# Optimization experiments

Measured on AMD Instinct MI355X. Metric: run time of the kernel, lower is better.

The kernel has to match this reference:

```python
import jax, jax.numpy as jnp
import numpy as np

C = 64          # out_C
IN_C = 2 * C    # in_C
B, H, W = 4, 64, 64


def conv_bn_relu(x, w, s, b):
    # 3x3 conv (stride 1, pad 1, no bias) + folded BatchNorm affine + ReLU
    y = jax.lax.conv_general_dilated(
        x, w, window_strides=(1, 1), padding=((1, 1), (1, 1)),
        dimension_numbers=("NCHW", "OIHW", "NCHW"))
    return jax.nn.relu(y * s[None, :, None, None] + b[None, :, None, None])


def attend(K, V, Q):
    # K, V, Q: [B, C, H, W]; mask = softmax(K^T Q) over last dim; out = V @ mask^T
    b, c, h, w = V.shape
    n = h * w
    Kf = K.reshape(b, c, n)
    Vf = V.reshape(b, c, n)
    Qf = Q.reshape(b, c, n)
    mask = jax.nn.softmax(jnp.einsum("bcn,bcm->bnm", Kf, Qf), axis=-1)  # [B,N,N]
    ref = jnp.einsum("bcn,bmn->bcm", Vf, mask)                          # V @ mask^T
    return ref.reshape(b, c, h, w)


def _conv_params(key, cin, cout):
    k1, k2, k3 = jax.random.split(key, 3)
    w = jax.random.normal(k1, (cout, cin, 3, 3), jnp.float32) * (1.0 / np.sqrt(cin * 9))
    s = jax.random.uniform(k2, (cout,), jnp.float32, 0.5, 1.5)   # folded BN scale
    bb = jax.random.normal(k3, (cout,), jnp.float32) * 0.1       # folded BN shift
    return w, s, bb


def setup_inputs() -> dict:
    key = jax.random.key(0)
    ks = jax.random.split(key, 9)
    x = jax.random.normal(ks[0], (B, C, H, W), jnp.float32)
    y = jax.random.normal(ks[1], (B, C, H, W), jnp.float32)
    q_w, q_s, q_b = _conv_params(ks[2], IN_C, C)
    rk_w, rk_s, rk_b = _conv_params(ks[3], C, C)
    rv_w, rv_s, rv_b = _conv_params(ks[4], C, C)
    ik_w, ik_s, ik_b = _conv_params(ks[5], C, C)
    iv_w, iv_s, iv_b = _conv_params(ks[6], C, C)
    sr_w, sr_s, sr_b = _conv_params(ks[7], IN_C, C)
    g1 = jax.random.normal(jax.random.fold_in(ks[8], 1), (1,), jnp.float32) * 0.1
    g2 = jax.random.normal(jax.random.fold_in(ks[8], 2), (1,), jnp.float32) * 0.1
    return dict(x=x, y=y,
                q_w=q_w, q_s=q_s, q_b=q_b,
                rk_w=rk_w, rk_s=rk_s, rk_b=rk_b,
                rv_w=rv_w, rv_s=rv_s, rv_b=rv_b,
                ik_w=ik_w, ik_s=ik_s, ik_b=ik_b,
                iv_w=iv_w, iv_s=iv_s, iv_b=iv_b,
                sr_w=sr_w, sr_s=sr_s, sr_b=sr_b,
                gamma1=g1, gamma2=g2)


def reference(x, y, q_w, q_s, q_b, rk_w, rk_s, rk_b, rv_w, rv_s, rv_b,
              ik_w, ik_s, ik_b, iv_w, iv_s, iv_b, sr_w, sr_s, sr_b,
              gamma1, gamma2):
    Q = conv_bn_relu(jnp.concatenate([x, y], axis=1), q_w, q_s, q_b)
    rgb_k = conv_bn_relu(x, rk_w, rk_s, rk_b)
    rgb_v = conv_bn_relu(x, rv_w, rv_s, rv_b)
    rgb_refine = gamma1[0] * attend(rgb_k, rgb_v, Q) + y
    inf_k = conv_bn_relu(y, ik_w, ik_s, ik_b)
    inf_v = conv_bn_relu(y, iv_w, iv_s, iv_b)
    inf_refine = gamma2[0] * attend(inf_k, inf_v, Q) + x
    out = conv_bn_relu(jnp.concatenate([rgb_refine, inf_refine], axis=1), sr_w, sr_s, sr_b)
    return out
```

## Files before the change

kernel.cpp:

```cpp
#include <hip/hip_runtime.h>
#include <hip/hip_bf16.h>

#define NPOS 4096
#define CD   64
#define NB   4
#define PADW 66
#define PADN (66*66)
#define NSEG 4
#define NT   (NPOS / NSEG / 64)
#define LOG2E 1.4426950408889634f

extern "C" __device__ float __ocml_exp2_f32(float);

typedef __bf16 bf16x8_t __attribute__((ext_vector_type(8)));
typedef float  f32x4_t  __attribute__((ext_vector_type(4)));

static __device__ __forceinline__ unsigned short f2bf(float f) {
    return __builtin_bit_cast(unsigned short, __float2bfloat16(f));
}

static __device__ __forceinline__ void gload_lds16(const void* g, void* l) {
    __builtin_amdgcn_global_load_lds(
        (const __attribute__((address_space(1))) void*)g,
        (__attribute__((address_space(3))) void*)l, 16, 0, 0);
}

static __device__ __forceinline__ unsigned cvtpk_bf16(float lo, float hi) {
    unsigned r;
    asm("v_cvt_pk_bf16_f32 %0, %1, %2" : "=v"(r) : "v"(lo), "v"(hi));
    return r;
}

__global__ __launch_bounds__(256) void prep_kernel(
    const float* __restrict__ x, const float* __restrict__ y,
    const float* __restrict__ qw, const float* __restrict__ rkw,
    const float* __restrict__ rvw, const float* __restrict__ ikw,
    const float* __restrict__ ivw, const float* __restrict__ srw,
    const float* __restrict__ qs, const float* __restrict__ rks,
    const float* __restrict__ rvs, const float* __restrict__ iks,
    const float* __restrict__ ivs, const float* __restrict__ srs,
    unsigned short* __restrict__ pads, unsigned short* __restrict__ Wf)
{
    const int bx = blockIdx.x;
    if (bx < 16) {
        unsigned short* p = pads + (size_t)bx * PADN * CD;
        const uint4 z = make_uint4(0, 0, 0, 0);
        for (int idx = threadIdx.x; idx < 260 * 8; idx += 256) {
            const int pi = idx >> 3, chn = idx & 7;
            int pos;
            if (pi < 66)       pos = pi;
            else if (pi < 132) pos = 65 * PADW + (pi - 66);
            else { const int rem = pi - 132;
                   pos = (1 + (rem >> 1)) * PADW + ((rem & 1) ? 65 : 0); }
            *(uint4*)(p + (size_t)pos * CD + chn * 8) = z;
        }
        return;
    }
    if (bx < 160) {
        const int f = bx - 16;
        const float* w; const float* s; int cin, local;
        if (f < 36)       { w = qw;  s = qs;  cin = 128; local = f; }
        else if (f < 54)  { w = rkw; s = rks; cin = 64;  local = f - 36; }
        else if (f < 72)  { w = rvw; s = rvs; cin = 64;  local = f - 54; }
        else if (f < 90)  { w = ikw; s = iks; cin = 64;  local = f - 72; }
        else if (f < 108) { w = ivw; s = ivs; cin = 64;  local = f - 90; }
        else              { w = srw; s = srs; cin = 128; local = f - 108; }
        const int src = (cin == 128) ? local / 18 : 0;
        const int rem = (cin == 128) ? local % 18 : local;
        const int tap = rem >> 1, kt = rem & 1;
        const int t = threadIdx.x, cot = t >> 6, l = t & 63;
        const int co = cot * 16 + (l & 15);
        const float kmul = ((f >= 36 && f < 54) || (f >= 72 && f < 90)) ? LOG2E : 1.0f;
        const float sc = s[co] * kmul;
        unsigned short us[8];
#pragma unroll
        for (int e = 0; e < 8; ++e) {
            const int ci = src * 64 + kt * 32 + ((l >> 4) * 8) + e;
            us[e] = f2bf(w[((size_t)co * cin + ci) * 9 + tap] * sc);
        }
        *(uint4*)(Wf + ((size_t)(f * 4 + cot) * 64 + l) * 8) = *(uint4*)us;
        return;
    }
    {
        const int idx = bx - 160;
        const int h = idx & 63, b = (idx >> 6) & 3, src = idx >> 8;
        const float* in = src ? y : x;
        unsigned short* out = pads + (size_t)src * NB * PADN * CD;
        __shared__ float t[64][65];
        const int tt = threadIdx.x;
        {
            const int ci = tt >> 2, w0 = (tt & 3) * 16;
            const float* p = in + ((size_t)b * 64 + ci) * NPOS + h * 64 + w0;
#pragma unroll
            for (int j = 0; j < 16; j += 4) {
                float4 v = *(const float4*)(p + j);
                t[ci][w0 + j] = v.x; t[ci][w0 + j + 1] = v.y;
                t[ci][w0 + j + 2] = v.z; t[ci][w0 + j + 3] = v.w;
            }
        }
        __syncthreads();
        const int w = tt >> 2, c0 = (tt & 3) * 16;
        unsigned short us[16];
#pragma unroll
        for (int j = 0; j < 16; ++j) us[j] = f2bf(t[c0 + j][w]);
        unsigned short* q = out + ((size_t)b * PADN + (h + 1) * PADW + (w + 1)) * CD + c0;
        *(uint4*)q = *(uint4*)us;
        *(uint4*)(q + 8) = *(uint4*)(us + 8);
    }
}

__global__ __launch_bounds__(256) void conv_mfma_kernel(
    const unsigned short* __restrict__ xpad, const unsigned short* __restrict__ ypad,
    const unsigned short* __restrict__ rpadR, const unsigned short* __restrict__ rpadI,
    const unsigned short* __restrict__ Wf,
    const float* __restrict__ qb, const float* __restrict__ rkb,
    const float* __restrict__ rvb, const float* __restrict__ ikb,
    const float* __restrict__ ivb, const float* __restrict__ srb,
    unsigned short* __restrict__ Qt, unsigned short* __restrict__ KtR,
    unsigned short* __restrict__ VR, unsigned short* __restrict__ KtI,
    unsigned short* __restrict__ VI, float* __restrict__ outf,
    int convid_base)
{
    const int conv = convid_base + (blockIdx.z >> 1);
    const int ch   = blockIdx.z & 1;
    const int hg = blockIdx.x, b = blockIdx.y;
    const unsigned short *in0, *in1; const float* bias;
    int nsrc, wfbase, layout; void* outp;
    switch (conv) {
        case 0:  in0 = xpad;  in1 = ypad;  nsrc = 2; wfbase = 0;   bias = qb;  outp = Qt;  layout = 0; break;
        case 1:  in0 = xpad;  in1 = 0;     nsrc = 1; wfbase = 36;  bias = rkb; outp = KtR; layout = 0; break;
        case 2:  in0 = xpad;  in1 = 0;     nsrc = 1; wfbase = 54;  bias = rvb; outp = VR;  layout = 1; break;
        case 3:  in0 = ypad;  in1 = 0;     nsrc = 1; wfbase = 72;  bias = ikb; outp = KtI; layout = 0; break;
        case 4:  in0 = ypad;  in1 = 0;     nsrc = 1; wfbase = 90;  bias = ivb; outp = VI;  layout = 1; break;
        default: in0 = rpadR; in1 = rpadI; nsrc = 2; wfbase = 108; bias = srb; outp = outf; layout = 2; break;
    }
    const float bmul = (conv == 1 || conv == 3) ? LOG2E : 1.0f;
    const int tid = threadIdx.x;
    const int lane = tid & 63, wv = tid >> 6;
    const int l15 = lane & 15, g = lane >> 4;
    const int rr = wv >> 1;
    const int wseg = (wv & 1) * 32;

    __shared__ unsigned short As[264 * 64];
    __shared__ unsigned short Wl[36 * 512];

    f32x4_t acc[2][2];
#pragma unroll
    for (int i = 0; i < 2; ++i)
#pragma unroll
        for (int j = 0; j < 2; ++j) acc[i][j] = (f32x4_t){0.f, 0.f, 0.f, 0.f};

    for (int src = 0; src < nsrc; ++src) {
        if (src) __syncthreads();
        const unsigned short* tsrc =
            (src ? in1 : in0) + ((size_t)b * PADN + (size_t)hg * 2 * PADW) * CD;
        for (int k = 0; k < 2112; k += 256) {
            const int idx = k + tid;
            if (idx < 2112) {
                const int s = (idx & ~7) | ((idx ^ (idx >> 3)) & 7);
                gload_lds16(tsrc + (size_t)s * 8, As + (size_t)(idx & ~63) * 8);
            }
        }
#pragma unroll
        for (int j = 0; j < 9; ++j) {
            const int slot = wv * 9 + j;
            const int fg = wfbase + src * 18 + (slot >> 1);
            gload_lds16(Wf + ((size_t)(fg * 4 + ch * 2 + (slot & 1)) * 64 + lane) * 8,
                        Wl + slot * 512);
        }
        __syncthreads();
#pragma unroll
        for (int ky = 0; ky < 3; ++ky) {
#pragma unroll
            for (int kx = 0; kx < 3; ++kx) {
#pragma unroll
                for (int kt = 0; kt < 2; ++kt) {
                    const int fj = (ky * 3 + kx) * 2 + kt;
                    bf16x8_t a[2];
#pragma unroll
                    for (int pf = 0; pf < 2; ++pf) {
                        const int P = (rr + ky) * 66 + wseg + pf * 16 + kx + l15;
                        const int q = (kt * 4 + g) ^ (P & 7);
                        a[pf] = *(const bf16x8_t*)(As + P * 64 + q * 8);
                    }
#pragma unroll
                    for (int cc = 0; cc < 2; ++cc) {
                        bf16x8_t wfr = *(const bf16x8_t*)(Wl + (size_t)(fj * 2 + cc) * 512 + lane * 8);
                        acc[0][cc] = __builtin_amdgcn_mfma_f32_16x16x32_bf16(a[0], wfr, acc[0][cc], 0, 0, 0);
                        acc[1][cc] = __builtin_amdgcn_mfma_f32_16x16x32_bf16(a[1], wfr, acc[1][cc], 0, 0, 0);
                    }
                }
            }
        }
    }

    const int hrow = hg * 2 + rr;
#pragma unroll
    for (int pf = 0; pf < 2; ++pf) {
        const int nb4 = hrow * 64 + wseg + pf * 16 + g * 4;
        if (layout == 0) {
            unsigned short* o = (unsigned short*)outp + (size_t)b * NPOS * CD;
#pragma unroll
            for (int cc = 0; cc < 2; ++cc) {
                const int co = (ch * 2 + cc) * 16 + l15;
                const float bv = bias[co] * bmul;
#pragma unroll
                for (int r = 0; r < 4; ++r)
                    o[(size_t)(nb4 + r) * CD + co] = f2bf(fmaxf(acc[pf][cc][r] + bv, 0.f));
            }
        } else if (layout == 1) {
            unsigned short* o = (unsigned short*)outp + (size_t)b * CD * NPOS;
#pragma unroll
            for (int cc = 0; cc < 2; ++cc) {
                const int cch = (ch * 2 + cc) * 16 + l15;
                const float bv = bias[cch];
                unsigned short us[4];
#pragma unroll
                for (int r = 0; r < 4; ++r) us[r] = f2bf(fmaxf(acc[pf][cc][r] + bv, 0.f));
                *(uint2*)(o + (size_t)cch * NPOS + nb4) = *(uint2*)us;
            }
        } else {
            float* o = (float*)outp + (size_t)b * CD * NPOS;
#pragma unroll
            for (int cc = 0; cc < 2; ++cc) {
                const int cch = (ch * 2 + cc) * 16 + l15;
                const float bv = bias[cch];
                f32x4_t v;
#pragma unroll
                for (int r = 0; r < 4; ++r) v[r] = fmaxf(acc[pf][cc][r] + bv, 0.f);
                *(f32x4_t*)(o + (size_t)cch * NPOS + nb4) = v;
            }
        }
    }
}

__global__ __launch_bounds__(256) void attn_kernel(
    const unsigned short* __restrict__ Qt,
    const unsigned short* __restrict__ KtR, const unsigned short* __restrict__ KtI,
    const unsigned short* __restrict__ VR,  const unsigned short* __restrict__ VI,
    float* __restrict__ Opart, float* __restrict__ ml)
{
    const int fid = blockIdx.x;
    const int att = fid & 1;
    const int b   = (fid >> 1) & 3;
    const int seg = (fid >> 3) & 3;
    const int mblk = fid >> 5;
    const int lane = threadIdx.x & 63, wv = threadIdx.x >> 6;
    const int l15 = lane & 15, g = lane >> 4;
    const int m0 = mblk * 64 + wv * 16;

    const unsigned short* Qb = Qt + (size_t)b * NPOS * CD;
    const unsigned short* Kb = (att ? KtI : KtR) + (size_t)b * NPOS * CD;
    const unsigned short* Vb = (att ? VI : VR) + (size_t)b * CD * NPOS;

    __shared__ unsigned short Qs[2][64 * 64];
    __shared__ unsigned short Vs[2][64 * 64];
    __shared__ unsigned short plds[4][16 * 68];
    unsigned short* pl = plds[wv];

    const bf16x8_t bK0 = *(const bf16x8_t*)&Kb[(size_t)(m0 + l15) * CD + g * 8];
    const bf16x8_t bK1 = *(const bf16x8_t*)&Kb[(size_t)(m0 + l15) * CD + 32 + g * 8];

    f32x4_t O[4];
#pragma unroll
    for (int i = 0; i < 4; ++i) O[i] = (f32x4_t){0.f, 0.f, 0.f, 0.f};
    float mrun = -3.0e38f, lsum = 0.f;

    const int csw = (lane & 7) ^ ((lane >> 3) & 7);
    const int sx = l15 & 7;
    const int nbase = seg * (NPOS / NSEG);

    const int rq = wv * 16 + (lane >> 3);
    const unsigned short* qsrc0 = Qb + (size_t)(nbase + rq) * CD + csw * 8;
    const unsigned short* qsrc1 = qsrc0 + (size_t)8 * CD;
    const unsigned short* vsrc0 = Vb + (size_t)rq * NPOS + nbase + csw * 8;
    const unsigned short* vsrc1 = vsrc0 + (size_t)8 * NPOS;
    unsigned short* qdst = &Qs[0][(wv * 16) * 64];
    unsigned short* vdst = &Vs[0][(wv * 16) * 64];

#define STAGE(buf, itv) do {                                                  \
        const size_t qo = (size_t)(itv) * (64 * CD);                          \
        const size_t vo = (size_t)(itv) * 64;                                 \
        gload_lds16(qsrc0 + qo, qdst + (buf) * 4096);                         \
        gload_lds16(qsrc1 + qo, qdst + (buf) * 4096 + 512);                   \
        gload_lds16(vsrc0 + vo, vdst + (buf) * 4096);                         \
        gload_lds16(vsrc1 + vo, vdst + (buf) * 4096 + 512);                   \
    } while (0)

    STAGE(0, 0);

    for (int it = 0; it < NT; ++it) {
        const int cur = it & 1;
        __syncthreads();
        if (it + 1 < NT) STAGE(cur ^ 1, it + 1);

        f32x4_t St[4];
        __builtin_amdgcn_s_setprio(1);
#pragma unroll
        for (int nt = 0; nt < 4; ++nt) {
            const unsigned short* qr = &Qs[cur][(nt * 16 + l15) * 64];
            bf16x8_t a0 = *(const bf16x8_t*)(qr + (g ^ sx) * 8);
            bf16x8_t a1 = *(const bf16x8_t*)(qr + ((4 + g) ^ sx) * 8);
            f32x4_t c = (f32x4_t){0.f, 0.f, 0.f, 0.f};
            c = __builtin_amdgcn_mfma_f32_16x16x32_bf16(a0, bK0, c, 0, 0, 0);
            c = __builtin_amdgcn_mfma_f32_16x16x32_bf16(a1, bK1, c, 0, 0, 0);
            St[nt] = c;
        }
        __builtin_amdgcn_s_setprio(0);

        float tmax = St[0][0];
#pragma unroll
        for (int nt = 0; nt < 4; ++nt) {
            tmax = fmaxf(fmaxf(tmax, St[nt][0]), St[nt][1]);
            tmax = fmaxf(fmaxf(tmax, St[nt][2]), St[nt][3]);
        }
        if (!__all(tmax <= mrun + 12.0f)) {
            float tr = fmaxf(tmax, __shfl_xor(tmax, 16));
            tr = fmaxf(tr, __shfl_xor(tr, 32));
            const float mnew = fmaxf(mrun, tr);
            const float corr = __builtin_amdgcn_exp2f(mrun - mnew);
            lsum *= corr;
#pragma unroll
            for (int i = 0; i < 4; ++i) {
                O[i][0] *= corr; O[i][1] *= corr; O[i][2] *= corr; O[i][3] *= corr;
            }
            mrun = mnew;
        }
        unsigned int pw[8];
#pragma unroll
        for (int nt = 0; nt < 4; ++nt) {
            float p0 = __builtin_amdgcn_exp2f(St[nt][0] - mrun);
            float p1 = __builtin_amdgcn_exp2f(St[nt][1] - mrun);
            float p2 = __builtin_amdgcn_exp2f(St[nt][2] - mrun);
            float p3 = __builtin_amdgcn_exp2f(St[nt][3] - mrun);
            lsum += (p0 + p1) + (p2 + p3);
            pw[nt * 2 + 0] = cvtpk_bf16(p0, p1);
            pw[nt * 2 + 1] = cvtpk_bf16(p2, p3);
        }
#pragma unroll
        for (int nt = 0; nt < 4; ++nt)
            *(uint2*)&pl[l15 * 68 + nt * 16 + g * 4] =
                make_uint2(pw[nt * 2], pw[nt * 2 + 1]);

        __builtin_amdgcn_s_setprio(1);
#pragma unroll
        for (int nc = 0; nc < 2; ++nc) {
            union { bf16x8_t v; uint2 d2[2]; } bp;
            bp.d2[0] = *(uint2*)&pl[l15 * 68 + nc * 32 + g * 8];
            bp.d2[1] = *(uint2*)&pl[l15 * 68 + nc * 32 + g * 8 + 4];
#pragma unroll
            for (int ct = 0; ct < 4; ++ct) {
                bf16x8_t av = *(const bf16x8_t*)
                    (&Vs[cur][(ct * 16 + l15) * 64 + (((nc * 4 + g) ^ sx) * 8)]);
                O[ct] = __builtin_amdgcn_mfma_f32_16x16x32_bf16(av, bp.v, O[ct], 0, 0, 0);
            }
        }
        __builtin_amdgcn_s_setprio(0);
    }

    float lred = lsum + __shfl_xor(lsum, 16);
    lred += __shfl_xor(lred, 32);
    float* Ob = Opart + ((((size_t)att * NB + b) * NSEG + seg) * NPOS) * CD;
    const int m = m0 + l15;
#pragma unroll
    for (int ct = 0; ct < 4; ++ct)
        *(f32x4_t*)(Ob + (size_t)m * CD + ct * 16 + g * 4) = O[ct];
    if (g == 0) {
        float* mlb = ml + ((((size_t)att * NB + b) * NSEG + seg) * NPOS + m) * 2;
        mlb[0] = mrun; mlb[1] = lred;
    }
#undef STAGE
}

__global__ __launch_bounds__(256) void combine_kernel(
    const float* __restrict__ Opart, const float* __restrict__ ml,
    const float* __restrict__ x, const float* __restrict__ y,
    const float* __restrict__ g1, const float* __restrict__ g2,
    unsigned short* __restrict__ rpadR, unsigned short* __restrict__ rpadI)
{
    const int mt = blockIdx.x, b = blockIdx.y, att = blockIdx.z;
    const float* resid = att ? x : y;
    const float gamma = att ? g2[0] : g1[0];
    unsigned short* rp = (att ? rpadI : rpadR) + (size_t)b * PADN * CD;
    __shared__ float t[64][17];
    const int tt = threadIdx.x;
    {
        const int c = tt >> 2, m4 = (tt & 3) * 4;
        const float4 v = *(const float4*)(resid + ((size_t)b * CD + c) * NPOS + mt * 16 + m4);
        t[c][m4] = v.x; t[c][m4 + 1] = v.y; t[c][m4 + 2] = v.z; t[c][m4 + 3] = v.w;
    }
    __syncthreads();
    const int c = tt & 63, mq = tt >> 6;
    const size_t ob = (((size_t)att * NB + b) * NSEG) * NPOS * CD;
    const size_t mb = (((size_t)att * NB + b) * NSEG) * NPOS;
#pragma unroll
    for (int p = 0; p < 4; ++p) {
        const int mloc = mq * 4 + p;
        const int m = mt * 16 + mloc;
        float mm[NSEG], llv[NSEG];
#pragma unroll
        for (int s = 0; s < NSEG; ++s) {
            mm[s] = ml[(mb + (size_t)s * NPOS + m) * 2];
            llv[s] = ml[(mb + (size_t)s * NPOS + m) * 2 + 1];
        }
        float M = mm[0];
#pragma unroll
        for (int s = 1; s < NSEG; ++s) M = fmaxf(M, mm[s]);
        float Ov = 0.f, L = 0.f;
#pragma unroll
        for (int s = 0; s < NSEG; ++s) {
            const float wgt = __ocml_exp2_f32(mm[s] - M);
            L += wgt * llv[s];
            Ov += wgt * Opart[ob + ((size_t)s * NPOS + m) * CD + c];
        }
        const float val = fmaf(gamma, Ov / L, t[c][mloc]);
        const int h = m >> 6, w_ = m & 63;
        rp[((size_t)((h + 1) * PADW) + (w_ + 1)) * CD + c] = f2bf(val);
    }
}

extern "C" void kernel_launch(void* const* d_in, const int* in_sizes, int n_in,
                              void* d_out, int out_size, void* d_ws, size_t ws_size,
                              hipStream_t stream)
{
    const float* x    = (const float*)d_in[0];
    const float* y    = (const float*)d_in[1];
    const float* q_w  = (const float*)d_in[2];
    const float* q_s  = (const float*)d_in[3];
    const float* q_b  = (const float*)d_in[4];
    const float* rk_w = (const float*)d_in[5];
    const float* rk_s = (const float*)d_in[6];
    const float* rk_b = (const float*)d_in[7];
    const float* rv_w = (const float*)d_in[8];
    const float* rv_s = (const float*)d_in[9];
    const float* rv_b = (const float*)d_in[10];
    const float* ik_w = (const float*)d_in[11];
    const float* ik_s = (const float*)d_in[12];
    const float* ik_b = (const float*)d_in[13];
    const float* iv_w = (const float*)d_in[14];
    const float* iv_s = (const float*)d_in[15];
    const float* iv_b = (const float*)d_in[16];
    const float* sr_w = (const float*)d_in[17];
    const float* sr_s = (const float*)d_in[18];
    const float* sr_b = (const float*)d_in[19];
    const float* g1   = (const float*)d_in[20];
    const float* g2   = (const float*)d_in[21];

    char* ws = (char*)d_ws;
    size_t off = 0;
    auto alloc = [&](size_t bytes) {
        void* p = ws + off; off += (bytes + 255) & ~(size_t)255; return p;
    };
    const size_t PADB = (size_t)NB * PADN * CD * 2;
    unsigned short* xpad  = (unsigned short*)alloc(PADB);
    unsigned short* ypad  = (unsigned short*)alloc(PADB);
    unsigned short* rpadR = (unsigned short*)alloc(PADB);
    unsigned short* rpadI = (unsigned short*)alloc(PADB);
    unsigned short* Qt  = (unsigned short*)alloc((size_t)NB * NPOS * CD * 2);
    unsigned short* KtR = (unsigned short*)alloc((size_t)NB * NPOS * CD * 2);
    unsigned short* KtI = (unsigned short*)alloc((size_t)NB * NPOS * CD * 2);
    unsigned short* VR  = (unsigned short*)alloc((size_t)NB * NPOS * CD * 2);
    unsigned short* VI  = (unsigned short*)alloc((size_t)NB * NPOS * CD * 2);
    unsigned short* Wf  = (unsigned short*)alloc((size_t)144 * 4 * 64 * 16);
    float* Opart = (float*)alloc((size_t)2 * NB * NSEG * NPOS * CD * 4);
    float* mlb   = (float*)alloc((size_t)2 * NB * NSEG * NPOS * 2 * 4);

    prep_kernel<<<dim3(672), 256, 0, stream>>>(
        x, y, q_w, rk_w, rv_w, ik_w, iv_w, sr_w,
        q_s, rk_s, rv_s, ik_s, iv_s, sr_s, xpad, Wf);
    conv_mfma_kernel<<<dim3(32, NB, 10), 256, 0, stream>>>(
        xpad, ypad, rpadR, rpadI, Wf,
        q_b, rk_b, rv_b, ik_b, iv_b, sr_b,
        Qt, KtR, VR, KtI, VI, nullptr, 0);
    conv_mfma_kernel<<<dim3(32, NB, 10), 256, 0, stream>>>(
        xpad, ypad, rpadR, rpadI, Wf,
        q_b, rk_b, rv_b, ik_b, iv_b, sr_b,
        Qt, KtR, VR, KtI, VI, nullptr, 0);
    attn_kernel<<<dim3(64 * NB * 2 * NSEG), 256, 0, stream>>>(
        Qt, KtR, KtI, VR, VI, Opart, mlb);
    combine_kernel<<<dim3(256, NB, 2), 256, 0, stream>>>(
        Opart, mlb, x, y, g1, g2, rpadR, rpadI);
    conv_mfma_kernel<<<dim3(32, NB, 2), 256, 0, stream>>>(
        xpad, ypad, rpadR, rpadI, Wf,
        q_b, rk_b, rv_b, ik_b, iv_b, sr_b,
        Qt, KtR, VR, KtI, VI, (float*)d_out, 5);
}
```

Measured before the change: 207.4 us.

## Switch attention to 32x32x16 MFMA with register-resident P and drop duplicate conv launch

The attention kernel moves from 16x16x32 MFMA tiles to 32x32x16 tiles. Each wave now covers 32 query columns, so the block count halves. The softmax probabilities are passed to the PV matmul through v_permlane32_swap in registers instead of a per-wave LDS round trip, which removes LDS writes, reads and the extra buffer. A duplicated conv launch that recomputed identical Q/K/V outputs is also removed. The cost is more accumulator registers under launch_bounds(256,4), which could cause spills or lower occupancy, and fewer blocks in flight.

```diff
diff --git a/kernel.cpp b/kernel.cpp
--- a/kernel.cpp
+++ b/kernel.cpp
@@ -14,6 +14,7 @@
 
 typedef __bf16 bf16x8_t __attribute__((ext_vector_type(8)));
 typedef float  f32x4_t  __attribute__((ext_vector_type(4)));
+typedef float  f32x16_t __attribute__((ext_vector_type(16)));
 
 static __device__ __forceinline__ unsigned short f2bf(float f) {
     return __builtin_bit_cast(unsigned short, __float2bfloat16(f));
@@ -234,7 +235,7 @@
     }
 }
 
-__global__ __launch_bounds__(256) void attn_kernel(
+__global__ __launch_bounds__(256, 4) void attn_kernel(
     const unsigned short* __restrict__ Qt,
     const unsigned short* __restrict__ KtR, const unsigned short* __restrict__ KtI,
     const unsigned short* __restrict__ VR,  const unsigned short* __restrict__ VI,
@@ -246,8 +247,8 @@
     const int seg = (fid >> 3) & 3;
     const int mblk = fid >> 5;
     const int lane = threadIdx.x & 63, wv = threadIdx.x >> 6;
-    const int l15 = lane & 15, g = lane >> 4;
-    const int m0 = mblk * 64 + wv * 16;
+    const int l31 = lane & 31, hi = lane >> 5;
+    const int m0w = mblk * 128 + wv * 32;
 
     const unsigned short* Qb = Qt + (size_t)b * NPOS * CD;
     const unsigned short* Kb = (att ? KtI : KtR) + (size_t)b * NPOS * CD;
@@ -255,19 +256,19 @@
 
     __shared__ unsigned short Qs[2][64 * 64];
     __shared__ unsigned short Vs[2][64 * 64];
-    __shared__ unsigned short plds[4][16 * 68];
-    unsigned short* pl = plds[wv];
-
-    const bf16x8_t bK0 = *(const bf16x8_t*)&Kb[(size_t)(m0 + l15) * CD + g * 8];
-    const bf16x8_t bK1 = *(const bf16x8_t*)&Kb[(size_t)(m0 + l15) * CD + 32 + g * 8];
-
-    f32x4_t O[4];
-#pragma unroll
-    for (int i = 0; i < 4; ++i) O[i] = (f32x4_t){0.f, 0.f, 0.f, 0.f};
+
+    const unsigned short* kbase = Kb + (size_t)(m0w + l31) * CD + hi * 8;
+    bf16x8_t fK[4];
+#pragma unroll
+    for (int kq = 0; kq < 4; ++kq)
+        fK[kq] = *(const bf16x8_t*)(kbase + kq * 16);
+
+    f32x16_t Oa, Ob2;
+#pragma unroll
+    for (int i = 0; i < 16; ++i) { Oa[i] = 0.f; Ob2[i] = 0.f; }
     float mrun = -3.0e38f, lsum = 0.f;
 
     const int csw = (lane & 7) ^ ((lane >> 3) & 7);
-    const int sx = l15 & 7;
     const int nbase = seg * (NPOS / NSEG);
 
     const int rq = wv * 16 + (lane >> 3);
@@ -289,83 +290,95 @@
 
     STAGE(0, 0);
 
+    const int r0x = l31 & 7;
+
     for (int it = 0; it < NT; ++it) {
         const int cur = it & 1;
         __syncthreads();
         if (it + 1 < NT) STAGE(cur ^ 1, it + 1);
 
-        f32x4_t St[4];
+        f32x16_t StA, StB;
+#pragma unroll
+        for (int i = 0; i < 16; ++i) { StA[i] = 0.f; StB[i] = 0.f; }
+        const unsigned short* qsl = Qs[cur];
         __builtin_amdgcn_s_setprio(1);
 #pragma unroll
-        for (int nt = 0; nt < 4; ++nt) {
-            const unsigned short* qr = &Qs[cur][(nt * 16 + l15) * 64];
-            bf16x8_t a0 = *(const bf16x8_t*)(qr + (g ^ sx) * 8);
-            bf16x8_t a1 = *(const bf16x8_t*)(qr + ((4 + g) ^ sx) * 8);
-            f32x4_t c = (f32x4_t){0.f, 0.f, 0.f, 0.f};
-            c = __builtin_amdgcn_mfma_f32_16x16x32_bf16(a0, bK0, c, 0, 0, 0);
-            c = __builtin_amdgcn_mfma_f32_16x16x32_bf16(a1, bK1, c, 0, 0, 0);
-            St[nt] = c;
+        for (int kq = 0; kq < 4; ++kq) {
+            const int chunk = ((kq << 1) | hi) ^ r0x;
+            bf16x8_t a0 = *(const bf16x8_t*)(qsl + (size_t)l31 * 64 + chunk * 8);
+            bf16x8_t a1 = *(const bf16x8_t*)(qsl + (size_t)(32 + l31) * 64 + chunk * 8);
+            StA = __builtin_amdgcn_mfma_f32_32x32x16_bf16(a0, fK[kq], StA, 0, 0, 0);
+            StB = __builtin_amdgcn_mfma_f32_32x32x16_bf16(a1, fK[kq], StB, 0, 0, 0);
         }
         __builtin_amdgcn_s_setprio(0);
 
-        float tmax = St[0][0];
-#pragma unroll
-        for (int nt = 0; nt < 4; ++nt) {
-            tmax = fmaxf(fmaxf(tmax, St[nt][0]), St[nt][1]);
-            tmax = fmaxf(fmaxf(tmax, St[nt][2]), St[nt][3]);
-        }
+        float tmax = StA[0];
+#pragma unroll
+        for (int r = 0; r < 16; r += 2)
+            tmax = fmaxf(fmaxf(tmax, StA[r]), StA[r + 1]);
+#pragma unroll
+        for (int r = 0; r < 16; r += 2)
+            tmax = fmaxf(fmaxf(tmax, StB[r]), StB[r + 1]);
         if (!__all(tmax <= mrun + 12.0f)) {
-            float tr = fmaxf(tmax, __shfl_xor(tmax, 16));
-            tr = fmaxf(tr, __shfl_xor(tr, 32));
+            const float tr = fmaxf(tmax, __shfl_xor(tmax, 32));
             const float mnew = fmaxf(mrun, tr);
             const float corr = __builtin_amdgcn_exp2f(mrun - mnew);
             lsum *= corr;
 #pragma unroll
-            for (int i = 0; i < 4; ++i) {
-                O[i][0] *= corr; O[i][1] *= corr; O[i][2] *= corr; O[i][3] *= corr;
-            }
+            for (int i = 0; i < 16; ++i) { Oa[i] *= corr; Ob2[i] *= corr; }
             mrun = mnew;
         }
-        unsigned int pw[8];
-#pragma unroll
-        for (int nt = 0; nt < 4; ++nt) {
-            float p0 = __builtin_amdgcn_exp2f(St[nt][0] - mrun);
-            float p1 = __builtin_amdgcn_exp2f(St[nt][1] - mrun);
-            float p2 = __builtin_amdgcn_exp2f(St[nt][2] - mrun);
-            float p3 = __builtin_amdgcn_exp2f(St[nt][3] - mrun);
-            lsum += (p0 + p1) + (p2 + p3);
-            pw[nt * 2 + 0] = cvtpk_bf16(p0, p1);
-            pw[nt * 2 + 1] = cvtpk_bf16(p2, p3);
-        }
-#pragma unroll
-        for (int nt = 0; nt < 4; ++nt)
-            *(uint2*)&pl[l15 * 68 + nt * 16 + g * 4] =
-                make_uint2(pw[nt * 2], pw[nt * 2 + 1]);
-
+
+        unsigned fr[4][4];
+#pragma unroll
+        for (int nb = 0; nb < 2; ++nb) {
+            float p[16];
+#pragma unroll
+            for (int r = 0; r < 16; ++r) {
+                p[r] = __builtin_amdgcn_exp2f((nb ? StB[r] : StA[r]) - mrun);
+                lsum += p[r];
+            }
+#pragma unroll
+            for (int hf = 0; hf < 2; ++hf) {
+                unsigned u0 = cvtpk_bf16(p[8 * hf + 0], p[8 * hf + 1]);
+                unsigned u1 = cvtpk_bf16(p[8 * hf + 2], p[8 * hf + 3]);
+                unsigned v0 = cvtpk_bf16(p[8 * hf + 4], p[8 * hf + 5]);
+                unsigned v1 = cvtpk_bf16(p[8 * hf + 6], p[8 * hf + 7]);
+                asm volatile("v_permlane32_swap_b32 %0, %1" : "+v"(u0), "+v"(v0));
+                asm volatile("v_permlane32_swap_b32 %0, %1" : "+v"(u1), "+v"(v1));
+                fr[nb * 2 + hf][0] = u0; fr[nb * 2 + hf][1] = u1;
+                fr[nb * 2 + hf][2] = v0; fr[nb * 2 + hf][3] = v1;
+            }
+        }
+
+        const unsigned short* vsl = Vs[cur];
         __builtin_amdgcn_s_setprio(1);
 #pragma unroll
-        for (int nc = 0; nc < 2; ++nc) {
-            union { bf16x8_t v; uint2 d2[2]; } bp;
-            bp.d2[0] = *(uint2*)&pl[l15 * 68 + nc * 32 + g * 8];
-            bp.d2[1] = *(uint2*)&pl[l15 * 68 + nc * 32 + g * 8 + 4];
-#pragma unroll
-            for (int ct = 0; ct < 4; ++ct) {
-                bf16x8_t av = *(const bf16x8_t*)
-                    (&Vs[cur][(ct * 16 + l15) * 64 + (((nc * 4 + g) ^ sx) * 8)]);
-                O[ct] = __builtin_amdgcn_mfma_f32_16x16x32_bf16(av, bp.v, O[ct], 0, 0, 0);
-            }
+        for (int nq = 0; nq < 4; ++nq) {
+            union { unsigned u[4]; bf16x8_t v; } bfr;
+            bfr.u[0] = fr[nq][0]; bfr.u[1] = fr[nq][1];
+            bfr.u[2] = fr[nq][2]; bfr.u[3] = fr[nq][3];
+            const int chunk = ((nq << 1) | hi) ^ r0x;
+            bf16x8_t av0 = *(const bf16x8_t*)(vsl + (size_t)l31 * 64 + chunk * 8);
+            bf16x8_t av1 = *(const bf16x8_t*)(vsl + (size_t)(32 + l31) * 64 + chunk * 8);
+            Oa  = __builtin_amdgcn_mfma_f32_32x32x16_bf16(av0, bfr.v, Oa, 0, 0, 0);
+            Ob2 = __builtin_amdgcn_mfma_f32_32x32x16_bf16(av1, bfr.v, Ob2, 0, 0, 0);
         }
         __builtin_amdgcn_s_setprio(0);
     }
 
-    float lred = lsum + __shfl_xor(lsum, 16);
-    lred += __shfl_xor(lred, 32);
-    float* Ob = Opart + ((((size_t)att * NB + b) * NSEG + seg) * NPOS) * CD;
-    const int m = m0 + l15;
-#pragma unroll
-    for (int ct = 0; ct < 4; ++ct)
-        *(f32x4_t*)(Ob + (size_t)m * CD + ct * 16 + g * 4) = O[ct];
-    if (g == 0) {
+    const float lred = lsum + __shfl_xor(lsum, 32);
+    const int m = m0w + l31;
+    float* Obase = Opart + ((((size_t)att * NB + b) * NSEG + seg) * NPOS + m) * CD;
+#pragma unroll
+    for (int q = 0; q < 4; ++q) {
+        f32x4_t w0, w1;
+#pragma unroll
+        for (int j = 0; j < 4; ++j) { w0[j] = Oa[4 * q + j]; w1[j] = Ob2[4 * q + j]; }
+        *(f32x4_t*)(Obase + 8 * q + 4 * hi) = w0;
+        *(f32x4_t*)(Obase + 32 + 8 * q + 4 * hi) = w1;
+    }
+    if (hi == 0) {
         float* mlb = ml + ((((size_t)att * NB + b) * NSEG + seg) * NPOS + m) * 2;
         mlb[0] = mrun; mlb[1] = lred;
     }
@@ -472,11 +485,7 @@
         xpad, ypad, rpadR, rpadI, Wf,
         q_b, rk_b, rv_b, ik_b, iv_b, sr_b,
         Qt, KtR, VR, KtI, VI, nullptr, 0);
-    conv_mfma_kernel<<<dim3(32, NB, 10), 256, 0, stream>>>(
-        xpad, ypad, rpadR, rpadI, Wf,
-        q_b, rk_b, rv_b, ik_b, iv_b, sr_b,
-        Qt, KtR, VR, KtI, VI, nullptr, 0);
-    attn_kernel<<<dim3(64 * NB * 2 * NSEG), 256, 0, stream>>>(
+    attn_kernel<<<dim3(32 * NB * 2 * NSEG), 256, 0, stream>>>(
         Qt, KtR, KtI, VR, VI, Opart, mlb);
     combine_kernel<<<dim3(256, NB, 2), 256, 0, stream>>>(
         Opart, mlb, x, y, g1, g2, rpadR, rpadI);
```

After: 177.6 us. -14.4%, faster.
